# Optimization experiments

Measured on AMD Instinct MI355X. Metric: run time of the kernel, lower is better.

## Reference

```python
import jax, jax.numpy as jnp
import numpy as np

NH = 12      # config.n_head
LEVEL = 2    # config.level -> Lmin = 4


def setup_inputs() -> dict:
    key = jax.random.key(0)
    ks = jax.random.split(key, 10)
    B, T, C = 1, 2048, 768
    hs = C // NH
    s = 0.02
    return {
        'x':   jax.random.normal(ks[0], (B, T, C), jnp.float32),
        'Wq':  jax.random.normal(ks[1], (C, C), jnp.float32) * s,
        'Wk':  jax.random.normal(ks[2], (C, C), jnp.float32) * s,
        'Wv':  jax.random.normal(ks[3], (C, C), jnp.float32) * s,
        'Wks': jax.random.normal(ks[4], (hs * hs, hs), jnp.float32) * s,
        'bks': jax.random.normal(ks[5], (hs,), jnp.float32) * s,
        'Wvs': jax.random.normal(ks[6], (hs * hs, hs), jnp.float32) * s,
        'bvs': jax.random.normal(ks[7], (hs,), jnp.float32) * s,
        'Wc':  jax.random.normal(ks[8], (C, C), jnp.float32) * s,
        'bc':  jax.random.normal(ks[9], (C,), jnp.float32) * s,
    }


def reference(x, Wq, Wk, Wv, Wks, bks, Wvs, bvs, Wc, bc):
    B, T, C = x.shape
    hs = C // NH
    Lmin = 2 ** LEVEL
    levelmax = int(np.log2(T))          # T is a power of two -> no ragged tails per level
    scale = hs ** -0.5

    # fla LinearAttention preprocess: bias-free projections + elu feature map (phi = elu+1)
    q = (jax.nn.elu(x @ Wq) + 1.0).reshape(B, T, NH, hs)
    k = (jax.nn.elu(x @ Wk) + 1.0).reshape(B, T, NH, hs)
    v = (x @ Wv).reshape(B, T, NH, hs)

    # per-position linear-attn state increments phi(k) v^T  [B,T,H,hs,hs]
    kv = jnp.einsum('bthi,bthj->bthij', k, v).reshape(B, T, NH, hs * hs)

    # tail features: running state within each block of Lmin (fused_recurrent final states
    # over the ragged per-position tail segments [t - t%Lmin, t])
    tail_feat = jnp.cumsum(kv.reshape(B, T // Lmin, Lmin, NH, hs * hs), axis=2)
    tail_feat = tail_feat.reshape(B, T, NH, hs * hs)

    # hierarchical set features: dyadic block sums at levels LEVEL..levelmax
    cur = kv.reshape(B, T // Lmin, Lmin, NH, hs * hs).sum(axis=2)
    feats, ends = [], []
    for l in range(LEVEL, levelmax + 1):
        n = T // (2 ** l)
        feats.append(cur)
        ends.append(np.arange(1, n + 1) * (2 ** l))   # exclusive end index of each set
        if n >= 2:
            cur = cur.reshape(B, n // 2, 2, NH, hs * hs).sum(axis=2)
    set_feat = jnp.concatenate(feats, axis=1)          # [B, S, H, hs*hs], S = 1023
    ends = np.concatenate(ends)                        # [S]
    mask = ends[None, :] <= (np.arange(T) + 1)[:, None]  # [T, S] causal set mask

    # k_mapping / v_mapping: Linear(hs^2 -> hs)
    K = set_feat @ Wks + bks        # [B,S,H,hs]
    V = set_feat @ Wvs + bvs
    K_tail = tail_feat @ Wks + bks  # [B,T,H,hs]
    V_tail = tail_feat @ Wvs + bvs

    logits = jnp.einsum('bthd,bshd->bhts', q, K) * scale      # [B,H,T,S]
    logits = jnp.where(mask[None, None], logits, jnp.float32(-1e30))
    tail_logit = jnp.einsum('bthd,bthd->bht', q, K_tail) * scale  # [B,H,T]
    att = jax.nn.softmax(jnp.concatenate([logits, tail_logit[..., None]], axis=-1), axis=-1)

    out = jnp.einsum('bhts,bshd->bhtd', att[..., :-1], V)
    out = out + att[..., -1:] * V_tail.transpose(0, 2, 1, 3)  # [B,H,T,hs]
    out = out.transpose(0, 2, 1, 3).reshape(B, T, C)
    return out @ Wc + bc
```

## Files before the change

kernel.cpp:

```cpp
#include <hip/hip_runtime.h>
#include <cstdint>

#define NHEAD 12
#define TLEN 2048
#define CDIM 768
#define NSETS 1023

typedef __attribute__((ext_vector_type(8))) _Float16 half8;
typedef __attribute__((ext_vector_type(2))) __fp16 fp16x2;
typedef __attribute__((ext_vector_type(8))) short short8;
typedef __attribute__((ext_vector_type(4))) float f32x4;

__device__ __forceinline__ float elu1(float x) { return x > 0.f ? x + 1.f : __expf(x); }

__device__ __forceinline__ unsigned pack2_bf16_trunc(float a, float b) {
    unsigned ua = __float_as_uint(a), ub = __float_as_uint(b);
    return __builtin_amdgcn_perm(ub, ua, 0x07060302);
}
__device__ __forceinline__ unsigned pack2_bf16_rne(float a, float b) {
    unsigned ua = __float_as_uint(a), ub = __float_as_uint(b);
    ua = ua + 0x7fff + ((ua >> 16) & 1);
    ub = ub + 0x7fff + ((ub >> 16) & 1);
    return (ub & 0xffff0000u) | (ua >> 16);
}
__device__ __forceinline__ short8 mk_short8(const unsigned* u) {
    union { unsigned w[4]; short8 s; } x;
    x.w[0] = u[0]; x.w[1] = u[1]; x.w[2] = u[2]; x.w[3] = u[3];
    return x.s;
}
__device__ __forceinline__ void split8_bf16(const float* f, short8& hi, short8& lo) {
    unsigned hp[4], lp[4];
    #pragma unroll
    for (int p = 0; p < 4; ++p) {
        float a = f[2 * p], b = f[2 * p + 1];
        unsigned ua = __float_as_uint(a), ub = __float_as_uint(b);
        hp[p] = __builtin_amdgcn_perm(ub, ua, 0x07060302);
        float ra = a - __uint_as_float(ua & 0xffff0000u);
        float rb = b - __uint_as_float(ub & 0xffff0000u);
        lp[p] = pack2_bf16_trunc(ra, rb);
    }
    hi = mk_short8(hp); lo = mk_short8(lp);
}
__device__ __forceinline__ void split8_f16(const float* f, half8& hi, half8& lo) {
    union { fp16x2 h2[4]; half8 h8; } uh, ul;
    #pragma unroll
    for (int jp = 0; jp < 4; ++jp) {
        float a = f[2 * jp], b = f[2 * jp + 1];
        fp16x2 hh = __builtin_amdgcn_cvt_pkrtz(a, b);
        uh.h2[jp] = hh;
        ul.h2[jp] = __builtin_amdgcn_cvt_pkrtz(a - (float)hh[0], b - (float)hh[1]);
    }
    hi = uh.h8; lo = ul.h8;
}

__global__ __launch_bounds__(256) void prep_w768x4(
    const float* __restrict__ Wq, const float* __restrict__ Wk,
    const float* __restrict__ Wv, const float* __restrict__ Wc4,
    _Float16* __restrict__ blobQKV, _Float16* __restrict__ blobC)
{
    const int g = blockIdx.x;
    const int sel = g / 2304;
    const float* W = sel == 0 ? Wq : (sel == 1 ? Wk : (sel == 2 ? Wv : Wc4));
    _Float16* blob = (sel < 3) ? (blobQKV + (size_t)sel * 589824) : blobC;
    const int idx = (g % 2304) * 256 + threadIdx.x;
    const int k = idx / 768, n = idx % 768;
    const int i = k >> 5, kl = k & 31;
    const int quad = kl >> 3, j = kl & 7;
    const int nsg = n >> 4, lane15 = n & 15;
    const int lane = quad * 16 + lane15;
    blob[((size_t)(i * 48 + nsg) * 64 + lane) * 8 + j] = (_Float16)W[idx];
}

__global__ __launch_bounds__(256) void prep_a_split(
    const float* __restrict__ A, _Float16* __restrict__ hi, _Float16* __restrict__ lo,
    int K)
{
    const int p = blockIdx.x * 256 + threadIdx.x;
    const int lane = p & 63, frag = p >> 6;
    const int k32n = K >> 5;
    const int m16 = frag / k32n, k32 = frag - m16 * k32n;
    const int row = m16 * 16 + (lane & 15);
    const int col = k32 * 32 + (lane >> 4) * 8;
    float f[8];
    *(float4*)&f[0] = *(const float4*)&A[(size_t)row * K + col];
    *(float4*)&f[4] = *(const float4*)&A[(size_t)row * K + col + 4];
    half8 h, l;
    split8_f16(f, h, l);
    *(half8*)&hi[(size_t)p * 8] = h;
    *(half8*)&lo[(size_t)p * 8] = l;
}

template<int QKV>
__global__ __launch_bounds__(256, 3) void gemm_frag(
    const _Float16* __restrict__ Ahi, const _Float16* __restrict__ Alo,
    const _Float16* __restrict__ Bblobs, const float* __restrict__ bias,
    float* __restrict__ outbase)
{
    const int nbx = QKV ? 18 : 6;
    const int cpx = QKV ? 72 : 24;
    int bid = blockIdx.x;
    bid = (bid & 7) * cpx + (bid >> 3);
    const int by  = bid / nbx;
    const int bxg = bid % nbx;
    const int which = QKV ? bxg / 6 : 0;
    const int bxm   = QKV ? bxg % 6 : bxg;
    const half8* __restrict__ Bc = (const half8*)(Bblobs + (size_t)which * 589824);
    float* __restrict__ Cmat = outbase + (size_t)which * ((size_t)TLEN * CDIM);
    const bool act = QKV ? (which < 2) : false;

    const int tid = threadIdx.x;
    const int wave = tid >> 6, lane = tid & 63;
    const int lane15 = lane & 15, quad = lane >> 4;
    const int m16b = by * 4;
    const int nsg0 = bxm * 8 + wave * 2;

    const half8* __restrict__ Ah = (const half8*)Ahi;
    const half8* __restrict__ Al = (const half8*)Alo;

    f32x4 acc[4][2];
    #pragma unroll
    for (int ms = 0; ms < 4; ++ms) {
        acc[ms][0] = (f32x4){0.f, 0.f, 0.f, 0.f};
        acc[ms][1] = (f32x4){0.f, 0.f, 0.f, 0.f};
    }

    const size_t aBase = ((size_t)m16b * 24) * 64 + lane;
    const size_t bBase = (size_t)nsg0 * 64 + lane;

    half8 bb[2], ah[4], al[4];
    bb[0] = Bc[bBase];
    bb[1] = Bc[bBase + 64];
    #pragma unroll
    for (int ms = 0; ms < 4; ++ms) {
        ah[ms] = Ah[aBase + (size_t)ms * (24 * 64)];
        al[ms] = Al[aBase + (size_t)ms * (24 * 64)];
    }

    for (int k32 = 0; k32 < 24; ++k32) {
        half8 bbn[2], ahn[4], aln[4];
        const bool more = (k32 + 1) < 24;
        if (more) {
            const size_t bo = bBase + (size_t)(k32 + 1) * (48 * 64);
            bbn[0] = Bc[bo]; bbn[1] = Bc[bo + 64];
            #pragma unroll
            for (int ms = 0; ms < 4; ++ms) {
                const size_t ao = aBase + (size_t)(k32 + 1) * 64 + (size_t)ms * (24 * 64);
                ahn[ms] = Ah[ao]; aln[ms] = Al[ao];
            }
        }
        #pragma unroll
        for (int ms = 0; ms < 4; ++ms) {
            acc[ms][0] = __builtin_amdgcn_mfma_f32_16x16x32_f16(ah[ms], bb[0], acc[ms][0], 0, 0, 0);
            acc[ms][1] = __builtin_amdgcn_mfma_f32_16x16x32_f16(ah[ms], bb[1], acc[ms][1], 0, 0, 0);
            acc[ms][0] = __builtin_amdgcn_mfma_f32_16x16x32_f16(al[ms], bb[0], acc[ms][0], 0, 0, 0);
            acc[ms][1] = __builtin_amdgcn_mfma_f32_16x16x32_f16(al[ms], bb[1], acc[ms][1], 0, 0, 0);
        }
        if (more) {
            bb[0] = bbn[0]; bb[1] = bbn[1];
            #pragma unroll
            for (int ms = 0; ms < 4; ++ms) { ah[ms] = ahn[ms]; al[ms] = aln[ms]; }
        }
    }

    #pragma unroll
    for (int ms = 0; ms < 4; ++ms)
        #pragma unroll
        for (int nb = 0; nb < 2; ++nb) {
            const int coln = (nsg0 + nb) * 16 + lane15;
            #pragma unroll
            for (int r = 0; r < 4; ++r) {
                const int row = m16b * 16 + ms * 16 + quad * 4 + r;
                float v = acc[ms][nb][r];
                if (!QKV) v += bias[coln];
                if (act) v = elu1(v);
                Cmat[(size_t)row * CDIM + coln] = v;
            }
        }
}

__global__ __launch_bounds__(256) void prep_w(
    const float* __restrict__ Wks, const float* __restrict__ Wvs,
    _Float16* __restrict__ Wblob)
{
    const int idx = blockIdx.x * 256 + threadIdx.x;
    const int kk = idx >> 7, n = idx & 127;
    float f = (n < 64) ? Wks[(size_t)kk * 64 + n] : Wvs[(size_t)kk * 64 + (n - 64)];
    const int i = kk >> 6, kl = kk & 63;
    const int ks = kl >> 5, quad = (kl >> 3) & 3, j = kl & 7;
    const int nsg = n >> 4, lane15 = n & 15;
    const int lane = quad * 16 + lane15;
    const size_t off = ((size_t)(((i * 2 + ks) * 8 + nsg)) * 64 + lane) * 8 + j;
    Wblob[off] = (_Float16)f;
}

__global__ __launch_bounds__(256, 2) void map_f16(
    const float* __restrict__ kbuf, const float* __restrict__ vbuf,
    const _Float16* __restrict__ Wblob,
    float* __restrict__ kkv, float* __restrict__ vvv)
{
    __shared__ unsigned kU[64][65];

    const int tid = threadIdx.x;
    const int p0 = blockIdx.x * 64;
    const int wave = tid >> 6, lane = tid & 63;
    const int lane15 = lane & 15, quad = lane >> 4;

    {
        const int row = tid >> 2, cb = (tid & 3) * 16;
        float f[16];
        *(float4*)&f[0]  = *(const float4*)&kbuf[(size_t)(p0 + row) * 64 + cb + 0];
        *(float4*)&f[4]  = *(const float4*)&kbuf[(size_t)(p0 + row) * 64 + cb + 4];
        *(float4*)&f[8]  = *(const float4*)&kbuf[(size_t)(p0 + row) * 64 + cb + 8];
        *(float4*)&f[12] = *(const float4*)&kbuf[(size_t)(p0 + row) * 64 + cb + 12];
        #pragma unroll
        for (int i = 0; i < 16; ++i) {
            union { fp16x2 h; unsigned u; } c;
            c.h = __builtin_amdgcn_cvt_pkrtz(f[i], f[i]);
            kU[row][cb + i] = c.u;
        }
    }

    half8 vrh[4][2];
    #pragma unroll
    for (int mh = 0; mh < 4; ++mh) {
        const size_t pbase = (size_t)(p0 + mh * 16 + lane15) * 64;
        #pragma unroll
        for (int ks = 0; ks < 2; ++ks) {
            float f[8];
            *(float4*)&f[0] = *(const float4*)&vbuf[pbase + ks * 32 + quad * 8];
            *(float4*)&f[4] = *(const float4*)&vbuf[pbase + ks * 32 + quad * 8 + 4];
            union { fp16x2 h2[4]; half8 h8; } u;
            #pragma unroll
            for (int jp = 0; jp < 4; ++jp)
                u.h2[jp] = __builtin_amdgcn_cvt_pkrtz(f[2 * jp], f[2 * jp + 1]);
            vrh[mh][ks] = u.h8;
        }
    }
    __syncthreads();

    const half8* __restrict__ Wc = (const half8*)Wblob;

    f32x4 acc[4][2];
    #pragma unroll
    for (int mh = 0; mh < 4; ++mh)
        #pragma unroll
        for (int nsl = 0; nsl < 2; ++nsl)
            acc[mh][nsl] = (f32x4){0.f, 0.f, 0.f, 0.f};

    half8 b0[2], b1[2], b2[2], b3[2];
    unsigned ka0[4], ka1[4], ka2[4], ka3[4];

    auto loadB = [&](half8* b, int s) {
        b[0] = Wc[(size_t)(s * 8 + 2 * wave) * 64 + lane];
        b[1] = Wc[(size_t)(s * 8 + 2 * wave + 1) * 64 + lane];
    };
    auto loadK = [&](unsigned* ka, int s) {
        const int i = s >> 1;
        #pragma unroll
        for (int mh = 0; mh < 4; ++mh) ka[mh] = kU[mh * 16 + lane15][i];
    };
    auto compute = [&](const half8* b, const unsigned* ka, int s) {
        const int ks = s & 1;
        #pragma unroll
        for (int mh = 0; mh < 4; ++mh) {
            union { unsigned u; fp16x2 h; } ku; ku.u = ka[mh];
            union { fp16x2 h2[4]; half8 h8; } va, ra;
            va.h8 = vrh[mh][ks];
            #pragma unroll
            for (int jp = 0; jp < 4; ++jp) ra.h2[jp] = ku.h * va.h2[jp];
            acc[mh][0] = __builtin_amdgcn_mfma_f32_16x16x32_f16(ra.h8, b[0], acc[mh][0], 0, 0, 0);
            acc[mh][1] = __builtin_amdgcn_mfma_f32_16x16x32_f16(ra.h8, b[1], acc[mh][1], 0, 0, 0);
        }
    };

    loadB(b0, 0); loadB(b1, 1); loadB(b2, 2); loadB(b3, 3);
    loadK(ka0, 0); loadK(ka1, 1); loadK(ka2, 2); loadK(ka3, 3);
    for (int s = 0; s < 128; s += 4) {
        const bool more = (s + 4) < 128;
        compute(b0, ka0, s);
        compute(b1, ka1, s + 1);
        if (more) { loadB(b0, s + 4); loadK(ka0, s + 4); loadB(b1, s + 5); loadK(ka1, s + 5); }
        compute(b2, ka2, s + 2);
        compute(b3, ka3, s + 3);
        if (more) { loadB(b2, s + 6); loadK(ka2, s + 6); loadB(b3, s + 7); loadK(ka3, s + 7); }
    }

    #pragma unroll
    for (int mh = 0; mh < 4; ++mh)
        #pragma unroll
        for (int nsl = 0; nsl < 2; ++nsl) {
            int n128 = (2 * wave + nsl) * 16 + lane15;
            float* dst = (n128 < 64) ? kkv : vvv;
            int col = n128 & 63;
            #pragma unroll
            for (int r = 0; r < 4; ++r) {
                int p = p0 + mh * 16 + quad * 4 + r;
                dst[(size_t)p * 64 + col] = acc[mh][nsl][r];
            }
        }
}

__global__ __launch_bounds__(256) void set_lower(
    const float* __restrict__ kkv, const float* __restrict__ vvv,
    const float* __restrict__ bks, const float* __restrict__ bvs,
    float* __restrict__ Kset, float* __restrict__ Vset,
    float* __restrict__ scrK, float* __restrict__ scrV,
    float* __restrict__ Kt, float* __restrict__ Vt)
{
    __shared__ float curK[63][64];
    __shared__ float curV[63][64];
    const int tid = threadIdx.x;
    const int col = tid & 63, grp = tid >> 6;
    const int h = blockIdx.x % NHEAD;
    const int c = blockIdx.x / NHEAD;
    const int t0 = c * 128;
    const float bk = bks[col], bv = bvs[col];

    for (int j = grp; j < 32; j += 4) {
        const size_t rbase = (size_t)(t0 + j * 4) * CDIM + h * 64 + col;
        const float* pk = kkv + rbase;
        const float* pv = vvv + rbase;
        float* ptK = Kt + rbase;
        float* ptV = Vt + rbase;
        float sk = bk, sv = bv;
        #pragma unroll
        for (int u = 0; u < 4; ++u) {
            sk += pk[(size_t)u * CDIM];
            sv += pv[(size_t)u * CDIM];
            ptK[(size_t)u * CDIM] = sk;
            ptV[(size_t)u * CDIM] = sv;
        }
        curK[j][col] = sk - bk; curV[j][col] = sv - bv;
        size_t o = ((size_t)(c * 32 + j) * NHEAD + h) * 64 + col;
        Kset[o] = sk; Vset[o] = sv;
    }
    __syncthreads();

    const int LBASE[6] = {0, 32, 48, 56, 60, 62};
    const int GBASE[6] = {0, 512, 768, 896, 960, 992};
    #pragma unroll
    for (int li = 1; li < 6; ++li) {
        const int ns = 32 >> li;
        for (int j = grp; j < ns; j += 4) {
            float sk = curK[LBASE[li - 1] + 2 * j][col] + curK[LBASE[li - 1] + 2 * j + 1][col];
            float sv = curV[LBASE[li - 1] + 2 * j][col] + curV[LBASE[li - 1] + 2 * j + 1][col];
            curK[LBASE[li] + j][col] = sk; curV[LBASE[li] + j][col] = sv;
            size_t o = ((size_t)(GBASE[li] + c * ns + j) * NHEAD + h) * 64 + col;
            Kset[o] = sk + bk; Vset[o] = sv + bv;
        }
        __syncthreads();
    }

    if (grp == 0) {
        scrK[((size_t)h * 16 + c) * 64 + col] = curK[62][col];
        scrV[((size_t)h * 16 + c) * 64 + col] = curV[62][col];
    }
}

__global__ __launch_bounds__(256) void set_upper(
    const float* __restrict__ scrK, const float* __restrict__ scrV,
    const float* __restrict__ bks, const float* __restrict__ bvs,
    float* __restrict__ Kset, float* __restrict__ Vset)
{
    __shared__ float cK[15][64], cV[15][64];
    const int h = blockIdx.x;
    const int tid = threadIdx.x, col = tid & 63, grp = tid >> 6;
    const float bk = bks[col], bv = bvs[col];

    for (int j = grp; j < 8; j += 4) {
        float sk = scrK[((size_t)h * 16 + 2 * j) * 64 + col] + scrK[((size_t)h * 16 + 2 * j + 1) * 64 + col];
        float sv = scrV[((size_t)h * 16 + 2 * j) * 64 + col] + scrV[((size_t)h * 16 + 2 * j + 1) * 64 + col];
        cK[j][col] = sk; cV[j][col] = sv;
        size_t o = ((size_t)(1008 + j) * NHEAD + h) * 64 + col;
        Kset[o] = sk + bk; Vset[o] = sv + bv;
    }
    __syncthreads();
    const int LB[4] = {0, 8, 12, 14};
    const int GB[4] = {1008, 1016, 1020, 1022};
    #pragma unroll
    for (int li = 1; li < 4; ++li) {
        const int ns = 8 >> li;
        for (int j = grp; j < ns; j += 4) {
            float sk = cK[LB[li - 1] + 2 * j][col] + cK[LB[li - 1] + 2 * j + 1][col];
            float sv = cV[LB[li - 1] + 2 * j][col] + cV[LB[li - 1] + 2 * j + 1][col];
            cK[LB[li] + j][col] = sk; cV[LB[li] + j][col] = sv;
            size_t o = ((size_t)(GB[li] + j) * NHEAD + h) * 64 + col;
            Kset[o] = sk + bk; Vset[o] = sv + bv;
        }
        __syncthreads();
    }
}

__global__ __launch_bounds__(256, 3) void attn_mfma(
    const float* __restrict__ qbuf, const float* __restrict__ Kset,
    const float* __restrict__ Vset, const float* __restrict__ Ktail,
    const float* __restrict__ Vtail,
    _Float16* __restrict__ atthi, _Float16* __restrict__ attlo)
{
    __shared__ int   sidAll[1024], sendAll[1024];
    __shared__ float sS[32][68];
    __shared__ unsigned sP[32][40];
    __shared__ unsigned vP[64][40];
    __shared__ float arowS[32];
    __shared__ float alS[32], ptS[32];

    const int tid = threadIdx.x;
    const int b   = 63 - (blockIdx.x / NHEAD);
    const int h   = blockIdx.x % NHEAD;
    const int T0  = b * 32;
    const int wave = tid >> 6, lane = tid & 63;
    const int lane15 = lane & 15, quad = lane >> 4;

    const int Tend = T0 + 32;
    const int LOFF[10] = {0, 512, 768, 896, 960, 992, 1008, 1016, 1020, 1022};
    int pfx[10], Vtot = 0;
    #pragma unroll
    for (int li = 0; li < 10; ++li) { pfx[li] = Vtot; Vtot += Tend >> (li + 2); }
    const int ntiles = (Vtot + 63) >> 6;

    for (int j = tid; j < 1024; j += 256) {
        int s_ = 0, e_ = 0x7fffffff;
        if (j < Vtot) {
            int li = 0;
            #pragma unroll
            for (int u = 1; u < 10; ++u) if (j >= pfx[u]) li = u;
            int idx = j - pfx[li];
            s_ = LOFF[li] + idx;
            e_ = (idx + 1) << (li + 2);
        }
        sidAll[j] = s_; sendAll[j] = e_;
    }

    short8 Qhi[2][2], Qlo[2][2];
    #pragma unroll
    for (int ms = 0; ms < 2; ++ms)
        #pragma unroll
        for (int kt = 0; kt < 2; ++kt) {
            const float* qp = qbuf + ((size_t)(T0 + ms * 16 + lane15) * NHEAD + h) * 64 + kt * 32 + quad * 8;
            float f[8];
            *(float4*)&f[0] = *(const float4*)qp;
            *(float4*)&f[4] = *(const float4*)(qp + 4);
            split8_bf16(f, Qhi[ms][kt], Qlo[ms][kt]);
        }

    __syncthreads();

    const int row = tid >> 3, part = tid & 7;
    float mreg = -1e30f, lreg = 0.f;

    f32x4 oacc[2];
    oacc[0] = (f32x4){0.f, 0.f, 0.f, 0.f};
    oacc[1] = (f32x4){0.f, 0.f, 0.f, 0.f};

    float4 Vr[4];
    float4 Kr[4];
    const int sp = tid >> 3, dd = (tid & 7) * 8;
    auto prefV = [&](int tile) {
        int sa = sidAll[tile * 64 + 2 * sp];
        int sb = sidAll[tile * 64 + 2 * sp + 1];
        const float* pa = Vset + ((size_t)sa * NHEAD + h) * 64 + dd;
        const float* pb = Vset + ((size_t)sb * NHEAD + h) * 64 + dd;
        Vr[0] = *(const float4*)pa; Vr[1] = *(const float4*)(pa + 4);
        Vr[2] = *(const float4*)pb; Vr[3] = *(const float4*)(pb + 4);
    };
    auto prefK = [&](int tile) {
        int sK = sidAll[tile * 64 + wave * 16 + lane15];
        const float* kp = Kset + ((size_t)sK * NHEAD + h) * 64 + quad * 8;
        Kr[0] = *(const float4*)kp;        Kr[1] = *(const float4*)(kp + 4);
        Kr[2] = *(const float4*)(kp + 32); Kr[3] = *(const float4*)(kp + 36);
    };
    prefV(0); prefK(0);

    for (int tile = 0; tile < ntiles; ++tile) {
        __syncthreads();

        {
            const float* va = (const float*)&Vr[0];
            const float* vb = (const float*)&Vr[2];
            #pragma unroll
            for (int i = 0; i < 8; ++i)
                vP[dd + i][sp] = pack2_bf16_rne(va[i], vb[i]);
        }

        short8 Khi[2], Klo[2];
        {
            float f[8];
            *(float4*)&f[0] = Kr[0]; *(float4*)&f[4] = Kr[1];
            split8_bf16(f, Khi[0], Klo[0]);
            *(float4*)&f[0] = Kr[2]; *(float4*)&f[4] = Kr[3];
            split8_bf16(f, Khi[1], Klo[1]);
        }

        f32x4 lacc[2];
        lacc[0] = (f32x4){0.f, 0.f, 0.f, 0.f};
        lacc[1] = (f32x4){0.f, 0.f, 0.f, 0.f};
        #pragma unroll
        for (int kt = 0; kt < 2; ++kt)
            #pragma unroll
            for (int ms = 0; ms < 2; ++ms) {
                lacc[ms] = __builtin_amdgcn_mfma_f32_16x16x32_bf16(Qhi[ms][kt], Khi[kt], lacc[ms], 0, 0, 0);
                lacc[ms] = __builtin_amdgcn_mfma_f32_16x16x32_bf16(Qlo[ms][kt], Khi[kt], lacc[ms], 0, 0, 0);
                lacc[ms] = __builtin_amdgcn_mfma_f32_16x16x32_bf16(Qhi[ms][kt], Klo[kt], lacc[ms], 0, 0, 0);
            }

        {
            const int sendv = sendAll[tile * 64 + wave * 16 + lane15];
            #pragma unroll
            for (int ms = 0; ms < 2; ++ms)
                #pragma unroll
                for (int r = 0; r < 4; ++r) {
                    int qrow = ms * 16 + quad * 4 + r;
                    bool ok = (T0 + qrow + 1) >= sendv;
                    sS[qrow][wave * 16 + lane15] = ok ? lacc[ms][r] * 0.125f : -1e30f;
                }
        }

        if (tile + 1 < ntiles) { prefV(tile + 1); prefK(tile + 1); }

        __syncthreads();

        {
            float4 a = *(float4*)&sS[row][part * 8];
            float4 c4 = *(float4*)&sS[row][part * 8 + 4];
            float mx = fmaxf(fmaxf(fmaxf(a.x, a.y), fmaxf(a.z, a.w)),
                             fmaxf(fmaxf(c4.x, c4.y), fmaxf(c4.z, c4.w)));
            mx = fmaxf(mx, __shfl_xor(mx, 1));
            mx = fmaxf(mx, __shfl_xor(mx, 2));
            mx = fmaxf(mx, __shfl_xor(mx, 4));
            float mnew = fmaxf(mreg, mx);
            float al = __expf(mreg - mnew);
            mreg = mnew;
            a.x = a.x > -1e29f ? __expf(a.x - mnew) : 0.f;
            a.y = a.y > -1e29f ? __expf(a.y - mnew) : 0.f;
            a.z = a.z > -1e29f ? __expf(a.z - mnew) : 0.f;
            a.w = a.w > -1e29f ? __expf(a.w - mnew) : 0.f;
            c4.x = c4.x > -1e29f ? __expf(c4.x - mnew) : 0.f;
            c4.y = c4.y > -1e29f ? __expf(c4.y - mnew) : 0.f;
            c4.z = c4.z > -1e29f ? __expf(c4.z - mnew) : 0.f;
            c4.w = c4.w > -1e29f ? __expf(c4.w - mnew) : 0.f;
            float sm = (a.x + a.y + a.z + a.w) + (c4.x + c4.y + c4.z + c4.w);
            sm += __shfl_xor(sm, 1);
            sm += __shfl_xor(sm, 2);
            sm += __shfl_xor(sm, 4);
            lreg = al * lreg + sm;
            unsigned w0 = pack2_bf16_rne(a.x, a.y);
            unsigned w1 = pack2_bf16_rne(a.z, a.w);
            unsigned w2 = pack2_bf16_rne(c4.x, c4.y);
            unsigned w3 = pack2_bf16_rne(c4.z, c4.w);
            *(uint4*)&sP[row][part * 4] = make_uint4(w0, w1, w2, w3);
            if (part == 0) arowS[row] = al;
        }

        __syncthreads();

        #pragma unroll
        for (int ms = 0; ms < 2; ++ms)
            #pragma unroll
            for (int r = 0; r < 4; ++r)
                oacc[ms][r] *= arowS[ms * 16 + quad * 4 + r];

        #pragma unroll
        for (int kt = 0; kt < 2; ++kt) {
            short8 Vf = *(short8*)&vP[wave * 16 + lane15][kt * 16 + quad * 4];
            #pragma unroll
            for (int ms = 0; ms < 2; ++ms) {
                short8 Pf = *(short8*)&sP[ms * 16 + lane15][kt * 16 + quad * 4];
                oacc[ms] = __builtin_amdgcn_mfma_f32_16x16x32_bf16(Pf, Vf, oacc[ms], 0, 0, 0);
            }
        }
    }

    {
        const float* qr = qbuf  + ((size_t)(T0 + row) * NHEAD + h) * 64 + part * 8;
        const float* kr = Ktail + ((size_t)(T0 + row) * NHEAD + h) * 64 + part * 8;
        float4 qa = *(const float4*)qr, qb = *(const float4*)(qr + 4);
        float4 ka = *(const float4*)kr, kb = *(const float4*)(kr + 4);
        float dp = qa.x * ka.x + qa.y * ka.y + qa.z * ka.z + qa.w * ka.w
                 + qb.x * kb.x + qb.y * kb.y + qb.z * kb.z + qb.w * kb.w;
        dp += __shfl_xor(dp, 1);
        dp += __shfl_xor(dp, 2);
        dp += __shfl_xor(dp, 4);
        float tl = dp * 0.125f;
        float mf = fmaxf(mreg, tl);
        float al = __expf(mreg - mf);
        float pt = __expf(tl - mf);
        float lf = al * lreg + pt;
        float inv = 1.f / lf;
        if (part == 0) { alS[row] = al * inv; ptS[row] = pt * inv; }
    }
    __syncthreads();

    #pragma unroll
    for (int ms = 0; ms < 2; ++ms)
        #pragma unroll
        for (int r = 0; r < 4; ++r) {
            int qrow = ms * 16 + quad * 4 + r;
            int col = wave * 16 + lane15;
            size_t base = ((size_t)(T0 + qrow) * NHEAD + h) * 64 + col;
            sS[qrow][col] = oacc[ms][r] * alS[qrow] + ptS[qrow] * Vtail[base];
        }
    __syncthreads();

    {
        const int kt = wave >> 1, msf = wave & 1;
        float f[8];
        *(float4*)&f[0] = *(const float4*)&sS[msf * 16 + lane15][kt * 32 + quad * 8];
        *(float4*)&f[4] = *(const float4*)&sS[msf * 16 + lane15][kt * 32 + quad * 8 + 4];
        half8 hh, ll;
        split8_f16(f, hh, ll);
        const size_t frag = (size_t)(b * 2 + msf) * 24 + (2 * h + kt);
        *(half8*)&atthi[(frag * 64 + lane) * 8] = hh;
        *(half8*)&attlo[(frag * 64 + lane) * 8] = ll;
    }
}

extern "C" void kernel_launch(void* const* d_in, const int* in_sizes, int n_in,
                              void* d_out, int out_size, void* d_ws, size_t ws_size,
                              hipStream_t stream)
{
    const float* x   = (const float*)d_in[0];
    const float* Wq  = (const float*)d_in[1];
    const float* Wk  = (const float*)d_in[2];
    const float* Wv  = (const float*)d_in[3];
    const float* Wks = (const float*)d_in[4];
    const float* bks = (const float*)d_in[5];
    const float* Wvs = (const float*)d_in[6];
    const float* bvs = (const float*)d_in[7];
    const float* Wc  = (const float*)d_in[8];
    const float* bc  = (const float*)d_in[9];
    float* out = (float*)d_out;

    float* ws = (float*)d_ws;
    const size_t TC = (size_t)TLEN * CDIM;
    float* q      = ws;
    float* k      = q + TC;
    float* v      = k + TC;
    float* kkv    = v + TC;
    float* vvv    = kkv + TC;
    float* Kt     = vvv + TC;
    float* Vt     = Kt + TC;
    float* Kset   = Vt + TC;
    float* Vset   = Kset + (size_t)NSETS * CDIM;
    float* attout = Vset + (size_t)NSETS * CDIM;
    _Float16* WblobMap = (_Float16*)attout;
    _Float16* blobQKV  = (_Float16*)(attout + 262144);
    float* scrK = attout + 1146880;
    float* scrV = scrK + 12 * 16 * 64;
    _Float16* blobC = (_Float16*)(attout + 1171456);
    _Float16* xhi = (_Float16*)kkv;
    _Float16* xlo = xhi + TC;
    _Float16* atthi = (_Float16*)vvv;
    _Float16* attlo = atthi + TC;

    prep_w768x4<<<4 * 2304, 256, 0, stream>>>(Wq, Wk, Wv, Wc, blobQKV, blobC);
    prep_w<<<(4096 * 128) / 256, 256, 0, stream>>>(Wks, Wvs, WblobMap);

    prep_a_split<<<(TLEN * CDIM / 8) / 256, 256, 0, stream>>>(x, xhi, xlo, CDIM);
    gemm_frag<1><<<576, 256, 0, stream>>>(xhi, xlo, blobQKV, nullptr, q);

    map_f16<<<(TLEN * NHEAD) / 64, 256, 0, stream>>>(k, v, WblobMap, kkv, vvv);

    set_lower<<<16 * NHEAD, 256, 0, stream>>>(kkv, vvv, bks, bvs, Kset, Vset, scrK, scrV, Kt, Vt);
    set_upper<<<NHEAD, 256, 0, stream>>>(scrK, scrV, bks, bvs, Kset, Vset);

    attn_mfma<<<(TLEN / 32) * NHEAD, 256, 0, stream>>>(q, Kset, Vset, Kt, Vt, atthi, attlo);

    gemm_frag<0><<<192, 256, 0, stream>>>(atthi, attlo, blobC, bc, out);
}
```

Baseline: 209.3 us.

## Merge prep kernels, emit fp16 K/V from QKV GEMM, double-buffer attention LDS

Three preprocessing kernels (weight blob packing, map weight packing, x hi/lo split) are merged into one launch to cut launch overhead. The QKV GEMM epilogue now writes K as duplicated fp16 pairs and V as fp16, so map_f16 only copies them and no longer converts fp32 inputs, which reduces memory traffic. The attention kernel packs set index and end into one shared array and double-buffers its shared tiles so one barrier per tile can be dropped. This raises shared memory use per block, which may lower occupancy, and the branchy merged prep kernel can diverge per block.

```diff
diff --git a/kernel.cpp b/kernel.cpp
--- a/kernel.cpp
+++ b/kernel.cpp
@@ -53,48 +53,60 @@
     hi = uh.h8; lo = ul.h8;
 }
 
-__global__ __launch_bounds__(256) void prep_w768x4(
+__global__ __launch_bounds__(256) void prep_all(
     const float* __restrict__ Wq, const float* __restrict__ Wk,
     const float* __restrict__ Wv, const float* __restrict__ Wc4,
-    _Float16* __restrict__ blobQKV, _Float16* __restrict__ blobC)
+    const float* __restrict__ Wks, const float* __restrict__ Wvs,
+    const float* __restrict__ x,
+    _Float16* __restrict__ blobQKV, _Float16* __restrict__ blobC,
+    _Float16* __restrict__ Wblob,
+    _Float16* __restrict__ xhi, _Float16* __restrict__ xlo)
 {
     const int g = blockIdx.x;
-    const int sel = g / 2304;
-    const float* W = sel == 0 ? Wq : (sel == 1 ? Wk : (sel == 2 ? Wv : Wc4));
-    _Float16* blob = (sel < 3) ? (blobQKV + (size_t)sel * 589824) : blobC;
-    const int idx = (g % 2304) * 256 + threadIdx.x;
-    const int k = idx / 768, n = idx % 768;
-    const int i = k >> 5, kl = k & 31;
-    const int quad = kl >> 3, j = kl & 7;
-    const int nsg = n >> 4, lane15 = n & 15;
-    const int lane = quad * 16 + lane15;
-    blob[((size_t)(i * 48 + nsg) * 64 + lane) * 8 + j] = (_Float16)W[idx];
-}
-
-__global__ __launch_bounds__(256) void prep_a_split(
-    const float* __restrict__ A, _Float16* __restrict__ hi, _Float16* __restrict__ lo,
-    int K)
-{
-    const int p = blockIdx.x * 256 + threadIdx.x;
-    const int lane = p & 63, frag = p >> 6;
-    const int k32n = K >> 5;
-    const int m16 = frag / k32n, k32 = frag - m16 * k32n;
-    const int row = m16 * 16 + (lane & 15);
-    const int col = k32 * 32 + (lane >> 4) * 8;
-    float f[8];
-    *(float4*)&f[0] = *(const float4*)&A[(size_t)row * K + col];
-    *(float4*)&f[4] = *(const float4*)&A[(size_t)row * K + col + 4];
-    half8 h, l;
-    split8_f16(f, h, l);
-    *(half8*)&hi[(size_t)p * 8] = h;
-    *(half8*)&lo[(size_t)p * 8] = l;
+    const int tid = threadIdx.x;
+    if (g < 9216) {
+        const int sel = g / 2304;
+        const float* W = sel == 0 ? Wq : (sel == 1 ? Wk : (sel == 2 ? Wv : Wc4));
+        _Float16* blob = (sel < 3) ? (blobQKV + (size_t)sel * 589824) : blobC;
+        const int idx = (g % 2304) * 256 + tid;
+        const int k = idx / 768, n = idx % 768;
+        const int i = k >> 5, kl = k & 31;
+        const int quad = kl >> 3, j = kl & 7;
+        const int nsg = n >> 4, lane15 = n & 15;
+        const int lane = quad * 16 + lane15;
+        blob[((size_t)(i * 48 + nsg) * 64 + lane) * 8 + j] = (_Float16)W[idx];
+    } else if (g < 9216 + 2048) {
+        const int idx = (g - 9216) * 256 + tid;
+        const int kk = idx >> 7, n = idx & 127;
+        float f = (n < 64) ? Wks[(size_t)kk * 64 + n] : Wvs[(size_t)kk * 64 + (n - 64)];
+        const int i = kk >> 6, kl = kk & 63;
+        const int ks = kl >> 5, quad = (kl >> 3) & 3, j = kl & 7;
+        const int nsg = n >> 4, lane15 = n & 15;
+        const int lane = quad * 16 + lane15;
+        const size_t off = ((size_t)(((i * 2 + ks) * 8 + nsg)) * 64 + lane) * 8 + j;
+        Wblob[off] = (_Float16)f;
+    } else {
+        const int p = (g - 11264) * 256 + tid;
+        const int lane = p & 63, frag = p >> 6;
+        const int m16 = frag / 24, k32 = frag - m16 * 24;
+        const int row = m16 * 16 + (lane & 15);
+        const int col = k32 * 32 + (lane >> 4) * 8;
+        float f[8];
+        *(float4*)&f[0] = *(const float4*)&x[(size_t)row * CDIM + col];
+        *(float4*)&f[4] = *(const float4*)&x[(size_t)row * CDIM + col + 4];
+        half8 h, l;
+        split8_f16(f, h, l);
+        *(half8*)&xhi[(size_t)p * 8] = h;
+        *(half8*)&xlo[(size_t)p * 8] = l;
+    }
 }
 
 template<int QKV>
 __global__ __launch_bounds__(256, 3) void gemm_frag(
     const _Float16* __restrict__ Ahi, const _Float16* __restrict__ Alo,
     const _Float16* __restrict__ Bblobs, const float* __restrict__ bias,
-    float* __restrict__ outbase)
+    float* __restrict__ outq, unsigned* __restrict__ kdup,
+    _Float16* __restrict__ v16)
 {
     const int nbx = QKV ? 18 : 6;
     const int cpx = QKV ? 72 : 24;
@@ -105,8 +117,6 @@
     const int which = QKV ? bxg / 6 : 0;
     const int bxm   = QKV ? bxg % 6 : bxg;
     const half8* __restrict__ Bc = (const half8*)(Bblobs + (size_t)which * 589824);
-    float* __restrict__ Cmat = outbase + (size_t)which * ((size_t)TLEN * CDIM);
-    const bool act = QKV ? (which < 2) : false;
 
     const int tid = threadIdx.x;
     const int wave = tid >> 6, lane = tid & 63;
@@ -170,31 +180,27 @@
             #pragma unroll
             for (int r = 0; r < 4; ++r) {
                 const int row = m16b * 16 + ms * 16 + quad * 4 + r;
-                float v = acc[ms][nb][r];
-                if (!QKV) v += bias[coln];
-                if (act) v = elu1(v);
-                Cmat[(size_t)row * CDIM + coln] = v;
+                float vv = acc[ms][nb][r];
+                if (!QKV) {
+                    outq[(size_t)row * CDIM + coln] = vv + bias[coln];
+                } else if (which == 0) {
+                    outq[(size_t)row * CDIM + coln] = elu1(vv);
+                } else if (which == 1) {
+                    float e = elu1(vv);
+                    union { fp16x2 h; unsigned u; } cc;
+                    cc.h = __builtin_amdgcn_cvt_pkrtz(e, e);
+                    kdup[(size_t)row * CDIM + coln] = cc.u;
+                } else {
+                    union { fp16x2 h; _Float16 f2[2]; } cc;
+                    cc.h = __builtin_amdgcn_cvt_pkrtz(vv, vv);
+                    v16[(size_t)row * CDIM + coln] = cc.f2[0];
+                }
             }
         }
 }
 
-__global__ __launch_bounds__(256) void prep_w(
-    const float* __restrict__ Wks, const float* __restrict__ Wvs,
-    _Float16* __restrict__ Wblob)
-{
-    const int idx = blockIdx.x * 256 + threadIdx.x;
-    const int kk = idx >> 7, n = idx & 127;
-    float f = (n < 64) ? Wks[(size_t)kk * 64 + n] : Wvs[(size_t)kk * 64 + (n - 64)];
-    const int i = kk >> 6, kl = kk & 63;
-    const int ks = kl >> 5, quad = (kl >> 3) & 3, j = kl & 7;
-    const int nsg = n >> 4, lane15 = n & 15;
-    const int lane = quad * 16 + lane15;
-    const size_t off = ((size_t)(((i * 2 + ks) * 8 + nsg)) * 64 + lane) * 8 + j;
-    Wblob[off] = (_Float16)f;
-}
-
 __global__ __launch_bounds__(256, 2) void map_f16(
-    const float* __restrict__ kbuf, const float* __restrict__ vbuf,
+    const unsigned* __restrict__ kdup, const _Float16* __restrict__ v16,
     const _Float16* __restrict__ Wblob,
     float* __restrict__ kkv, float* __restrict__ vvv)
 {
@@ -207,17 +213,15 @@
 
     {
         const int row = tid >> 2, cb = (tid & 3) * 16;
-        float f[16];
-        *(float4*)&f[0]  = *(const float4*)&kbuf[(size_t)(p0 + row) * 64 + cb + 0];
-        *(float4*)&f[4]  = *(const float4*)&kbuf[(size_t)(p0 + row) * 64 + cb + 4];
-        *(float4*)&f[8]  = *(const float4*)&kbuf[(size_t)(p0 + row) * 64 + cb + 8];
-        *(float4*)&f[12] = *(const float4*)&kbuf[(size_t)(p0 + row) * 64 + cb + 12];
-        #pragma unroll
-        for (int i = 0; i < 16; ++i) {
-            union { fp16x2 h; unsigned u; } c;
-            c.h = __builtin_amdgcn_cvt_pkrtz(f[i], f[i]);
-            kU[row][cb + i] = c.u;
-        }
+        const unsigned* src = &kdup[(size_t)(p0 + row) * 64 + cb];
+        uint4 a0 = *(const uint4*)(src + 0);
+        uint4 a1 = *(const uint4*)(src + 4);
+        uint4 a2 = *(const uint4*)(src + 8);
+        uint4 a3 = *(const uint4*)(src + 12);
+        *(uint4*)&kU[row][cb + 0]  = a0;
+        *(uint4*)&kU[row][cb + 4]  = a1;
+        *(uint4*)&kU[row][cb + 8]  = a2;
+        *(uint4*)&kU[row][cb + 12] = a3;
     }
 
     half8 vrh[4][2];
@@ -225,16 +229,8 @@
     for (int mh = 0; mh < 4; ++mh) {
         const size_t pbase = (size_t)(p0 + mh * 16 + lane15) * 64;
         #pragma unroll
-        for (int ks = 0; ks < 2; ++ks) {
-            float f[8];
-            *(float4*)&f[0] = *(const float4*)&vbuf[pbase + ks * 32 + quad * 8];
-            *(float4*)&f[4] = *(const float4*)&vbuf[pbase + ks * 32 + quad * 8 + 4];
-            union { fp16x2 h2[4]; half8 h8; } u;
-            #pragma unroll
-            for (int jp = 0; jp < 4; ++jp)
-                u.h2[jp] = __builtin_amdgcn_cvt_pkrtz(f[2 * jp], f[2 * jp + 1]);
-            vrh[mh][ks] = u.h8;
-        }
+        for (int ks = 0; ks < 2; ++ks)
+            vrh[mh][ks] = *(const half8*)&v16[pbase + ks * 32 + quad * 8];
     }
     __syncthreads();
 
@@ -397,11 +393,11 @@
     const float* __restrict__ Vtail,
     _Float16* __restrict__ atthi, _Float16* __restrict__ attlo)
 {
-    __shared__ int   sidAll[1024], sendAll[1024];
-    __shared__ float sS[32][68];
-    __shared__ unsigned sP[32][40];
-    __shared__ unsigned vP[64][40];
-    __shared__ float arowS[32];
+    __shared__ unsigned ssAll[1024];
+    __shared__ float sS[2][32][68];
+    __shared__ unsigned sP[2][32][40];
+    __shared__ unsigned vP[2][64][40];
+    __shared__ float arowS[2][32];
     __shared__ float alS[32], ptS[32];
 
     const int tid = threadIdx.x;
@@ -419,16 +415,15 @@
     const int ntiles = (Vtot + 63) >> 6;
 
     for (int j = tid; j < 1024; j += 256) {
-        int s_ = 0, e_ = 0x7fffffff;
+        unsigned pk = (4095u << 16);
         if (j < Vtot) {
             int li = 0;
             #pragma unroll
             for (int u = 1; u < 10; ++u) if (j >= pfx[u]) li = u;
             int idx = j - pfx[li];
-            s_ = LOFF[li] + idx;
-            e_ = (idx + 1) << (li + 2);
-        }
-        sidAll[j] = s_; sendAll[j] = e_;
+            pk = (unsigned)(LOFF[li] + idx) | ((unsigned)((idx + 1) << (li + 2)) << 16);
+        }
+        ssAll[j] = pk;
     }
 
     short8 Qhi[2][2], Qlo[2][2];
@@ -456,15 +451,15 @@
     float4 Kr[4];
     const int sp = tid >> 3, dd = (tid & 7) * 8;
     auto prefV = [&](int tile) {
-        int sa = sidAll[tile * 64 + 2 * sp];
-        int sb = sidAll[tile * 64 + 2 * sp + 1];
+        int sa = (int)(ssAll[tile * 64 + 2 * sp] & 0xffffu);
+        int sb = (int)(ssAll[tile * 64 + 2 * sp + 1] & 0xffffu);
         const float* pa = Vset + ((size_t)sa * NHEAD + h) * 64 + dd;
         const float* pb = Vset + ((size_t)sb * NHEAD + h) * 64 + dd;
         Vr[0] = *(const float4*)pa; Vr[1] = *(const float4*)(pa + 4);
         Vr[2] = *(const float4*)pb; Vr[3] = *(const float4*)(pb + 4);
     };
     auto prefK = [&](int tile) {
-        int sK = sidAll[tile * 64 + wave * 16 + lane15];
+        int sK = (int)(ssAll[tile * 64 + wave * 16 + lane15] & 0xffffu);
         const float* kp = Kset + ((size_t)sK * NHEAD + h) * 64 + quad * 8;
         Kr[0] = *(const float4*)kp;        Kr[1] = *(const float4*)(kp + 4);
         Kr[2] = *(const float4*)(kp + 32); Kr[3] = *(const float4*)(kp + 36);
@@ -472,14 +467,14 @@
     prefV(0); prefK(0);
 
     for (int tile = 0; tile < ntiles; ++tile) {
-        __syncthreads();
+        const int c = tile & 1;
 
         {
             const float* va = (const float*)&Vr[0];
             const float* vb = (const float*)&Vr[2];
             #pragma unroll
             for (int i = 0; i < 8; ++i)
-                vP[dd + i][sp] = pack2_bf16_rne(va[i], vb[i]);
+                vP[c][dd + i][sp] = pack2_bf16_rne(va[i], vb[i]);
         }
 
         short8 Khi[2], Klo[2];
@@ -504,14 +499,14 @@
             }
 
         {
-            const int sendv = sendAll[tile * 64 + wave * 16 + lane15];
+            const int sendv = (int)(ssAll[tile * 64 + wave * 16 + lane15] >> 16);
             #pragma unroll
             for (int ms = 0; ms < 2; ++ms)
                 #pragma unroll
                 for (int r = 0; r < 4; ++r) {
                     int qrow = ms * 16 + quad * 4 + r;
                     bool ok = (T0 + qrow + 1) >= sendv;
-                    sS[qrow][wave * 16 + lane15] = ok ? lacc[ms][r] * 0.125f : -1e30f;
+                    sS[c][qrow][wave * 16 + lane15] = ok ? lacc[ms][r] * 0.125f : -1e30f;
                 }
         }
 
@@ -520,8 +515,8 @@
         __syncthreads();
 
         {
-            float4 a = *(float4*)&sS[row][part * 8];
-            float4 c4 = *(float4*)&sS[row][part * 8 + 4];
+            float4 a = *(float4*)&sS[c][row][part * 8];
+            float4 c4 = *(float4*)&sS[c][row][part * 8 + 4];
             float mx = fmaxf(fmaxf(fmaxf(a.x, a.y), fmaxf(a.z, a.w)),
                              fmaxf(fmaxf(c4.x, c4.y), fmaxf(c4.z, c4.w)));
             mx = fmaxf(mx, __shfl_xor(mx, 1));
@@ -547,8 +542,8 @@
             unsigned w1 = pack2_bf16_rne(a.z, a.w);
             unsigned w2 = pack2_bf16_rne(c4.x, c4.y);
             unsigned w3 = pack2_bf16_rne(c4.z, c4.w);
-            *(uint4*)&sP[row][part * 4] = make_uint4(w0, w1, w2, w3);
-            if (part == 0) arowS[row] = al;
+            *(uint4*)&sP[c][row][part * 4] = make_uint4(w0, w1, w2, w3);
+            if (part == 0) arowS[c][row] = al;
         }
 
         __syncthreads();
@@ -557,14 +552,14 @@
         for (int ms = 0; ms < 2; ++ms)
             #pragma unroll
             for (int r = 0; r < 4; ++r)
-                oacc[ms][r] *= arowS[ms * 16 + quad * 4 + r];
+                oacc[ms][r] *= arowS[c][ms * 16 + quad * 4 + r];
 
         #pragma unroll
         for (int kt = 0; kt < 2; ++kt) {
-            short8 Vf = *(short8*)&vP[wave * 16 + lane15][kt * 16 + quad * 4];
+            short8 Vf = *(short8*)&vP[c][wave * 16 + lane15][kt * 16 + quad * 4];
             #pragma unroll
             for (int ms = 0; ms < 2; ++ms) {
-                short8 Pf = *(short8*)&sP[ms * 16 + lane15][kt * 16 + quad * 4];
+                short8 Pf = *(short8*)&sP[c][ms * 16 + lane15][kt * 16 + quad * 4];
                 oacc[ms] = __builtin_amdgcn_mfma_f32_16x16x32_bf16(Pf, Vf, oacc[ms], 0, 0, 0);
             }
         }
@@ -597,15 +592,15 @@
             int qrow = ms * 16 + quad * 4 + r;
             int col = wave * 16 + lane15;
             size_t base = ((size_t)(T0 + qrow) * NHEAD + h) * 64 + col;
-            sS[qrow][col] = oacc[ms][r] * alS[qrow] + ptS[qrow] * Vtail[base];
+            sS[0][qrow][col] = oacc[ms][r] * alS[qrow] + ptS[qrow] * Vtail[base];
         }
     __syncthreads();
 
     {
         const int kt = wave >> 1, msf = wave & 1;
         float f[8];
-        *(float4*)&f[0] = *(const float4*)&sS[msf * 16 + lane15][kt * 32 + quad * 8];
-        *(float4*)&f[4] = *(const float4*)&sS[msf * 16 + lane15][kt * 32 + quad * 8 + 4];
+        *(float4*)&f[0] = *(const float4*)&sS[0][msf * 16 + lane15][kt * 32 + quad * 8];
+        *(float4*)&f[4] = *(const float4*)&sS[0][msf * 16 + lane15][kt * 32 + quad * 8 + 4];
         half8 hh, ll;
         split8_f16(f, hh, ll);
         const size_t frag = (size_t)(b * 2 + msf) * 24 + (2 * h + kt);
@@ -649,21 +644,22 @@
     _Float16* blobC = (_Float16*)(attout + 1171456);
     _Float16* xhi = (_Float16*)kkv;
     _Float16* xlo = xhi + TC;
+    unsigned*  kdup = (unsigned*)k;
+    _Float16*  v16  = (_Float16*)v;
     _Float16* atthi = (_Float16*)vvv;
     _Float16* attlo = atthi + TC;
 
-    prep_w768x4<<<4 * 2304, 256, 0, stream>>>(Wq, Wk, Wv, Wc, blobQKV, blobC);
-    prep_w<<<(4096 * 128) / 256, 256, 0, stream>>>(Wks, Wvs, WblobMap);
-
-    prep_a_split<<<(TLEN * CDIM / 8) / 256, 256, 0, stream>>>(x, xhi, xlo, CDIM);
-    gemm_frag<1><<<576, 256, 0, stream>>>(xhi, xlo, blobQKV, nullptr, q);
-
-    map_f16<<<(TLEN * NHEAD) / 64, 256, 0, stream>>>(k, v, WblobMap, kkv, vvv);
+    prep_all<<<9216 + 2048 + 768, 256, 0, stream>>>(
+        Wq, Wk, Wv, Wc, Wks, Wvs, x, blobQKV, blobC, WblobMap, xhi, xlo);
+
+    gemm_frag<1><<<576, 256, 0, stream>>>(xhi, xlo, blobQKV, nullptr, q, kdup, v16);
+
+    map_f16<<<(TLEN * NHEAD) / 64, 256, 0, stream>>>(kdup, v16, WblobMap, kkv, vvv);
 
     set_lower<<<16 * NHEAD, 256, 0, stream>>>(kkv, vvv, bks, bvs, Kset, Vset, scrK, scrV, Kt, Vt);
     set_upper<<<NHEAD, 256, 0, stream>>>(scrK, scrV, bks, bvs, Kset, Vset);
 
     attn_mfma<<<(TLEN / 32) * NHEAD, 256, 0, stream>>>(q, Kset, Vset, Kt, Vt, atthi, attlo);
 
-    gemm_frag<0><<<192, 256, 0, stream>>>(atthi, attlo, blobC, bc, out);
-}
+    gemm_frag<0><<<192, 256, 0, stream>>>(atthi, attlo, blobC, bc, out, nullptr, nullptr);
+}
```

New measurement: 204.4 us. -2.3%, faster.
